# Kernel tuning notes

Measured on AMD Instinct MI355X. Metric: run time of the kernel, lower is better.

Reference implementation:

```python
import jax, jax.numpy as jnp
import numpy as np

DN = ('NCHW', 'OIHW', 'NCHW')

def conv3x3(x, w):
    # stride-1, SAME padding, no bias (matches build_conv_layer(..., 3, stride=1, padding='same', bias=False))
    return jax.lax.conv_general_dilated(x, w, window_strides=(1, 1), padding='SAME', dimension_numbers=DN)

def setup_inputs() -> dict:
    key = jax.random.key(0)
    k1, k2, k3, k4 = jax.random.split(key, 4)
    B, C, H, W = 4, 256, 64, 64
    inputs = jax.random.normal(k1, (B, C, H, W), dtype=jnp.float32)
    ref = jax.random.normal(k2, (B, C, H, W), dtype=jnp.float32)
    # xavier-uniform-ish conv weights, [O, I, kH, kW]
    fan = C * 9
    lim = np.sqrt(6.0 / (fan + fan)).astype(np.float32)
    w1 = jax.random.uniform(k3, (C, C, 3, 3), dtype=jnp.float32, minval=-lim, maxval=lim)
    w2 = jax.random.uniform(k4, (C, C, 3, 3), dtype=jnp.float32, minval=-lim, maxval=lim)
    gamma = jnp.float32(0.5)
    return {'inputs': inputs, 'ref': ref, 'w1': w1, 'w2': w2, 'gamma': gamma}

def reference(inputs, ref, w1, w2, gamma):
    # Faithful to source: x0 = relu(conv1(inputs)) is computed then immediately
    # overwritten by a view of x1 (a bug in the original), so inputs only
    # contributes its shape. We execute the dead conv for FLOP parity.
    _dead = jax.nn.relu(conv3x3(inputs, w1))
    x1 = jax.nn.relu(conv3x3(ref, w1))            # [B, C, H, W]
    B, C, H, W = x1.shape
    q = x1.transpose(0, 2, 3, 1).reshape(B, H * W, C)   # [B, HW, C]
    k = x1.reshape(B, C, H * W)                          # [B, C, HW]
    scores = jnp.einsum('bnc,bcm->bnm', q, k)            # [B, HW, HW]
    corr = jax.nn.softmax(scores, axis=1)                # softmax over dim=1 (atypical axis)
    v = jax.nn.relu(conv3x3(ref, w2)).reshape(B, C, H * W)  # [B, C, HW]
    A = jnp.einsum('bcn,bnm->bcm', v, corr).reshape(inputs.shape)
    return A * gamma + ref
```

## Files before the change

kernel.cpp:

```cpp
#include <hip/hip_runtime.h>
#include <math.h>

#define CDIM 256
#define NSEQ 4096
#define HWDIM 64
#define PPIX 4356

typedef unsigned short u16;
typedef __attribute__((ext_vector_type(8))) short bf16x8;
typedef __attribute__((ext_vector_type(4))) float f32x4;
typedef __attribute__((ext_vector_type(16))) float f32x16;

__device__ __forceinline__ u16 f2bf(float f) {
    unsigned u = __float_as_uint(f);
    unsigned r = (u + 0x7FFFu + ((u >> 16) & 1u)) >> 16;
    return (u16)r;
}

__device__ __forceinline__ void gload_lds16(const u16* g, u16* l) {
    __builtin_amdgcn_global_load_lds(
        (const __attribute__((address_space(1))) unsigned int*)g,
        (__attribute__((address_space(3))) unsigned int*)l, 16, 0, 0);
}

__global__ __launch_bounds__(256)
void pad_transpose_kernel(const float* __restrict__ x, u16* __restrict__ padded)
{
    __shared__ float lds[64 * 65];
    const int tid = threadIdx.x;
    const int y = blockIdx.x, c0 = blockIdx.y << 6, b = blockIdx.z;
    #pragma unroll
    for (int i = 0; i < 16; ++i) {
        int f = tid + (i << 8);
        int c = f >> 6, xx = f & 63;
        lds[c * 65 + xx] = x[(((size_t)(b * CDIM + c0 + c)) * HWDIM + y) * HWDIM + xx];
    }
    __syncthreads();
    #pragma unroll
    for (int i = 0; i < 2; ++i) {
        int f = tid + (i << 8);
        int xx = f >> 3, c8 = f & 7;
        union { u16 h[8]; float4 v; } pk;
        #pragma unroll
        for (int j = 0; j < 8; ++j) pk.h[j] = f2bf(lds[(c8 * 8 + j) * 65 + xx]);
        *(float4*)&padded[((size_t)b * PPIX + (y + 1) * 66 + (xx + 1)) * CDIM + c0 + (c8 << 3)] = pk.v;
    }
}

__global__ __launch_bounds__(256)
void w_prepack_kernel(const float* __restrict__ w, u16* __restrict__ wk)
{
    int t = (blockIdx.x << 8) + threadIdx.x;
    const float* wp = w + (size_t)t * 9;
    #pragma unroll
    for (int j = 0; j < 9; ++j) wk[j * 65536 + t] = f2bf(wp[j]);
}

template <bool OA>
__global__ __launch_bounds__(256)
void conv_mfma_kernel(const u16* __restrict__ padded, const u16* __restrict__ wk,
                      u16* __restrict__ out)
{
    __shared__ alignas(16) u16 Xs[64 * 64];
    __shared__ alignas(16) u16 Ws[128 * 64];

    const int tid = threadIdx.x;
    const int lane = tid & 63, wv = tid >> 6;
    const int lr = lane & 15, lg = lane >> 4;
    const int cb = blockIdx.x << 7;
    const int y0 = blockIdx.y;
    const int b = blockIdx.z;

    constexpr int MF = OA ? 4 : 2;
    constexpr int NF = OA ? 2 : 4;
    f32x4 acc[MF][NF] = {};

    for (int t = 0; t < 36; ++t) {
        const int kyx = t >> 2, cib = (t & 3) << 6;
        const int ky = kyx / 3, kx = kyx - ky * 3;
        __syncthreads();
        #pragma unroll
        for (int i = 0; i < 2; ++i) {
            int f = tid + (i << 8);
            int r = f >> 3, c8 = f & 7;
            int pp = (y0 + ky) * 66 + r + kx;
            float4 v = *(const float4*)&padded[((size_t)b * PPIX + pp) * CDIM + cib + (c8 << 3)];
            *(float4*)&Xs[(r << 6) + ((c8 << 3) ^ ((r & 7) << 3))] = v;
        }
        #pragma unroll
        for (int i = 0; i < 4; ++i) {
            int f = tid + (i << 8);
            int r = f >> 3, c8 = f & 7;
            float4 v = *(const float4*)&wk[((size_t)kyx << 16) + (size_t)(cb + r) * 256 + cib + (c8 << 3)];
            *(float4*)&Ws[(r << 6) + ((c8 << 3) ^ ((r & 7) << 3))] = v;
        }
        __syncthreads();
        #pragma unroll
        for (int kk = 0; kk < 2; ++kk) {
            const int ca = ((kk << 5) + (lg << 3)) ^ ((lr & 7) << 3);
            if constexpr (OA) {
                bf16x8 a[4], bb[2];
                #pragma unroll
                for (int mf = 0; mf < 4; ++mf)
                    a[mf] = *(const bf16x8*)&Xs[((mf * 16 + lr) << 6) + ca];
                #pragma unroll
                for (int nf = 0; nf < 2; ++nf)
                    bb[nf] = *(const bf16x8*)&Ws[((wv * 32 + nf * 16 + lr) << 6) + ca];
                #pragma unroll
                for (int mf = 0; mf < 4; ++mf)
                    #pragma unroll
                    for (int nf = 0; nf < 2; ++nf)
                        acc[mf][nf] = __builtin_amdgcn_mfma_f32_16x16x32_bf16(a[mf], bb[nf], acc[mf][nf], 0, 0, 0);
            } else {
                bf16x8 a[2], bb[4];
                #pragma unroll
                for (int mf = 0; mf < 2; ++mf)
                    a[mf] = *(const bf16x8*)&Ws[((wv * 32 + mf * 16 + lr) << 6) + ca];
                #pragma unroll
                for (int nf = 0; nf < 4; ++nf)
                    bb[nf] = *(const bf16x8*)&Xs[((nf * 16 + lr) << 6) + ca];
                #pragma unroll
                for (int mf = 0; mf < 2; ++mf)
                    #pragma unroll
                    for (int nf = 0; nf < 4; ++nf)
                        acc[mf][nf] = __builtin_amdgcn_mfma_f32_16x16x32_bf16(a[mf], bb[nf], acc[mf][nf], 0, 0, 0);
            }
        }
    }

    const int m0 = y0 << 6;
    if constexpr (OA) {
        #pragma unroll
        for (int mf = 0; mf < 4; ++mf)
            #pragma unroll
            for (int nf = 0; nf < 2; ++nf) {
                int nb = m0 + mf * 16 + lg * 4;
                int co = cb + wv * 32 + nf * 16 + lr;
                union { u16 h[4]; uint2 v; } pk;
                #pragma unroll
                for (int j = 0; j < 4; ++j) pk.h[j] = f2bf(fmaxf(acc[mf][nf][j], 0.f));
                *(uint2*)&out[((size_t)(b * CDIM + co)) * NSEQ + nb] = pk.v;
            }
    } else {
        #pragma unroll
        for (int mf = 0; mf < 2; ++mf)
            #pragma unroll
            for (int nf = 0; nf < 4; ++nf) {
                int cob = cb + wv * 32 + mf * 16 + lg * 4;
                int n = m0 + nf * 16 + lr;
                union { u16 h[4]; uint2 v; } pk;
                #pragma unroll
                for (int j = 0; j < 4; ++j) pk.h[j] = f2bf(fmaxf(acc[mf][nf][j], 0.f));
                *(uint2*)&out[((size_t)(b * NSEQ + n)) * CDIM + cob] = pk.v;
            }
    }
}

__global__ __launch_bounds__(256)
void rownorm_kernel(const u16* __restrict__ XT, float* __restrict__ rn2,
                    float* __restrict__ bmax)
{
    __shared__ float wmax[4];
    const int tid = threadIdx.x;
    const int lane = tid & 63, wv = tid >> 6;
    const int row = (blockIdx.x << 2) + wv;
    const u16* xp = &XT[(size_t)row * CDIM + (lane << 2)];
    uint2 v = *(const uint2*)xp;
    float s = 0.f;
    #pragma unroll
    for (int j = 0; j < 4; ++j) {
        unsigned hu = (j & 1) ? ((&v.x)[j >> 1] >> 16) : ((&v.x)[j >> 1] & 0xFFFFu);
        float x = __uint_as_float(hu << 16);
        s += x * x;
    }
    #pragma unroll
    for (int off = 1; off < 64; off <<= 1) s += __shfl_xor(s, off);
    if (lane == 0) {
        rn2[row] = s;
        wmax[wv] = s;
    }
    __syncthreads();
    if (tid == 0)
        bmax[blockIdx.x] = fmaxf(fmaxf(wmax[0], wmax[1]), fmaxf(wmax[2], wmax[3]));
}

__global__ __launch_bounds__(256)
void maxred_kernel(const float* __restrict__ bmax, float* __restrict__ maxrn2)
{
    __shared__ float wred[4];
    const int tid = threadIdx.x;
    const int lane = tid & 63, wv = tid >> 6;
    const int b = blockIdx.x;
    float m = 0.f;
    #pragma unroll
    for (int i = 0; i < 4; ++i)
        m = fmaxf(m, bmax[(b << 10) + (i << 8) + tid]);
    #pragma unroll
    for (int off = 1; off < 64; off <<= 1) m = fmaxf(m, __shfl_xor(m, off));
    if (lane == 0) wred[wv] = m;
    __syncthreads();
    if (tid == 0)
        maxrn2[b] = fmaxf(fmaxf(wred[0], wred[1]), fmaxf(wred[2], wred[3]));
}

#define M_TILE 128
#define NC 64
#define NCHUNKS 32

#define KS_OFF 0
#define VS_OFF 32768
#define P_OFF  65536

__device__ __forceinline__ void stage_chunk(const u16* __restrict__ XT, const u16* __restrict__ Vn,
                                            u16* Kb, u16* Vb, int b, int n0, int wv, int lane)
{
    #pragma unroll
    for (int i = 0; i < 4; ++i) {
        int f = ((i << 3) + wv) << 6;
        int fl = f + lane;
        int r = fl >> 5;
        int gsw = (fl & 31) ^ (r & 15);
        gload_lds16(&XT[(size_t)(b * NSEQ + n0 + r) * CDIM + (gsw << 3)], Kb + (f << 3));
    }
    #pragma unroll
    for (int i = 0; i < 4; ++i) {
        int f = ((i << 3) + wv) << 6;
        int fl = f + lane;
        int r = fl >> 3;
        int gsw = (fl & 7) ^ (r & 7);
        gload_lds16(&Vn[(size_t)(b * CDIM + r) * NSEQ + n0 + (gsw << 3)], Vb + (f << 3));
    }
}

__global__ __launch_bounds__(512, 2)
void attn_part_kernel(const u16* __restrict__ XT, const u16* __restrict__ Vn,
                      const float* __restrict__ rn2, const float* __restrict__ maxrn2,
                      float* __restrict__ o0, u16* __restrict__ o1,
                      float* __restrict__ lsum)
{
    __shared__ alignas(16) u16 smem[73728];
    u16* Ps = smem + P_OFF;

    const int tid = threadIdx.x;
    const int lane = tid & 63;
    const int wv = tid >> 6;
    const int l31 = lane & 31;
    const int hi = lane >> 5;
    const int bh = blockIdx.x;
    const int b = bh >> 1, h = bh & 1;
    const int m0 = blockIdx.y * M_TILE;
    const int nbase = h * (NSEQ / 2);

    const int qt = wv & 3;
    const int kh = wv >> 2;
    const int qa = qt * 32 + l31;
    const int qsel = wv & 1;
    const int csel = wv >> 1;

    const float mq = sqrtf(rn2[(size_t)b * NSEQ + m0 + qa]) * sqrtf(maxrn2[b]);

    bf16x8 qreg[16];
    {
        const u16* qrow = &XT[(size_t)(b * NSEQ + m0 + qa) * CDIM + (hi << 3)];
        #pragma unroll
        for (int ks = 0; ks < 16; ++ks)
            qreg[ks] = *(const bf16x8*)(qrow + (ks << 4));
    }

    f32x16 o[2][2] = {};
    float lrun = 0.f;

    stage_chunk(XT, Vn, smem + KS_OFF, smem + VS_OFF, b, nbase, wv, lane);
    __syncthreads();

    int cur = 0;
    for (int ci = 0; ci < NCHUNKS; ++ci) {
        if (ci + 1 < NCHUNKS)
            stage_chunk(XT, Vn, smem + KS_OFF + (cur ^ 1) * 16384,
                        smem + VS_OFF + (cur ^ 1) * 16384,
                        b, nbase + (ci + 1) * NC, wv, lane);

        const u16* Kc = smem + KS_OFF + cur * 16384;
        const u16* Vc = smem + VS_OFF + cur * 16384;

        f32x16 s = {};
        {
            const int krow = kh * 32 + l31;
            const u16* kbase = &Kc[krow << 8];
            const int ksw = krow & 15;
            #pragma unroll
            for (int ks = 0; ks < 16; ++ks) {
                bf16x8 ka = *(const bf16x8*)&kbase[(((ks << 1) + hi) ^ ksw) << 3];
                s = __builtin_amdgcn_mfma_f32_32x32x16_bf16(ka, qreg[ks], s, 0, 0, 0);
            }
        }

        float p[16];
        float ps = 0.f;
        #pragma unroll
        for (int r = 0; r < 16; ++r) { p[r] = __expf(s[r] - mq); ps += p[r]; }
        ps += __shfl_xor(ps, 32);
        lrun += ps;

        {
            const int swz = qa & 7;
            #pragma unroll
            for (int r4 = 0; r4 < 4; ++r4) {
                union { u16 h4[4]; uint2 v; } pk;
                pk.h4[0] = f2bf(p[r4 * 4 + 0]); pk.h4[1] = f2bf(p[r4 * 4 + 1]);
                pk.h4[2] = f2bf(p[r4 * 4 + 2]); pk.h4[3] = f2bf(p[r4 * 4 + 3]);
                int g = (kh << 2) + r4;
                *(uint2*)&Ps[(qa << 6) + (((g ^ swz) << 3) | (hi << 2))] = pk.v;
            }
        }
        __syncthreads();

        {
            const int q0 = ((qsel << 1) + 0) * 32 + l31;
            const int q1 = ((qsel << 1) + 1) * 32 + l31;
            const int c0 = ((csel << 1) + 0) * 32 + l31;
            const int c1 = ((csel << 1) + 1) * 32 + l31;
            #pragma unroll
            for (int ks = 0; ks < 4; ++ks) {
                const int gp = (ks << 1) + hi;
                bf16x8 pb0 = *(const bf16x8*)&Ps[(q0 << 6) + ((gp ^ (q0 & 7)) << 3)];
                bf16x8 pb1 = *(const bf16x8*)&Ps[(q1 << 6) + ((gp ^ (q1 & 7)) << 3)];
                bf16x8 va0 = *(const bf16x8*)&Vc[(c0 << 6) + ((gp ^ (c0 & 7)) << 3)];
                bf16x8 va1 = *(const bf16x8*)&Vc[(c1 << 6) + ((gp ^ (c1 & 7)) << 3)];
                o[0][0] = __builtin_amdgcn_mfma_f32_32x32x16_bf16(va0, pb0, o[0][0], 0, 0, 0);
                o[0][1] = __builtin_amdgcn_mfma_f32_32x32x16_bf16(va1, pb0, o[0][1], 0, 0, 0);
                o[1][0] = __builtin_amdgcn_mfma_f32_32x32x16_bf16(va0, pb1, o[1][0], 0, 0, 0);
                o[1][1] = __builtin_amdgcn_mfma_f32_32x32x16_bf16(va1, pb1, o[1][1], 0, 0, 0);
            }
        }

        __syncthreads();
        cur ^= 1;
    }

    if (lane < 32)
        lsum[(size_t)(((h * 2 + kh) * 4 + b)) * NSEQ + m0 + qa] = lrun;

    #pragma unroll
    for (int qi = 0; qi < 2; ++qi) {
        const int q = m0 + ((qsel << 1) + qi) * 32 + l31;
        #pragma unroll
        for (int cj = 0; cj < 2; ++cj) {
            #pragma unroll
            for (int reg = 0; reg < 16; ++reg) {
                int c = ((csel << 1) + cj) * 32 + (reg & 3) + ((reg >> 2) << 3) + (hi << 2);
                size_t oi = ((size_t)(b * CDIM + c)) * NSEQ + q;
                if (h == 0) o0[oi] = o[qi][cj][reg];
                else        o1[oi] = f2bf(o[qi][cj][reg]);
            }
        }
    }
}

__global__ __launch_bounds__(256)
void merge_kernel(float* __restrict__ out, const u16* __restrict__ o1,
                  const float* __restrict__ lsum, const float* __restrict__ ref,
                  const float* __restrict__ gptr)
{
    const int f = (blockIdx.x << 8) + threadIdx.x;
    const int n4 = f & 1023;
    const int c = (f >> 10) & 255;
    const int b = f >> 18;
    const float g = gptr[0];

    float4 p0 = ((const float4*)out)[f];
    uint2 q1 = *(const uint2*)&o1[((size_t)(b * CDIM + c)) * NSEQ + (n4 << 2)];
    float4 rf = ((const float4*)ref)[f];

    float res[4];
    #pragma unroll
    for (int j = 0; j < 4; ++j) {
        int row = (n4 << 2) + j;
        float l = lsum[(size_t)(0 * 4 + b) * NSEQ + row]
                + lsum[(size_t)(1 * 4 + b) * NSEQ + row]
                + lsum[(size_t)(2 * 4 + b) * NSEQ + row]
                + lsum[(size_t)(3 * 4 + b) * NSEQ + row];
        float rl = 1.0f / l;
        float v0 = ((const float*)&p0)[j];
        unsigned hu = ((j & 1) ? ((&q1.x)[j >> 1] >> 16) : ((&q1.x)[j >> 1] & 0xFFFFu));
        float v1 = __uint_as_float(hu << 16);
        float a = (v0 + v1) * rl;
        res[j] = g * a + ((const float*)&rf)[j];
    }
    ((float4*)out)[f] = *(float4*)res;
}

extern "C" void kernel_launch(void* const* d_in, const int* in_sizes, int n_in,
                              void* d_out, int out_size, void* d_ws, size_t ws_size,
                              hipStream_t stream)
{
    const float* ref = (const float*)d_in[1];
    const float* w1  = (const float*)d_in[2];
    const float* w2  = (const float*)d_in[3];
    const float* gma = (const float*)d_in[4];
    float* out = (float*)d_out;

    u16* XT     = (u16*)d_ws;
    u16* Vn     = XT + (size_t)4 * NSEQ * CDIM;
    u16* padded = Vn + (size_t)4 * NSEQ * CDIM;
    u16* wk1    = padded + (size_t)4 * PPIX * CDIM;
    u16* wk2    = wk1 + (size_t)9 * 65536;
    u16*   o1     = padded;
    float* lsum   = (float*)wk1;
    float* rn2    = (float*)wk2;
    float* bmax   = rn2 + 16384;
    float* maxrn2 = bmax + 4096;

    hipMemsetAsync(padded, 0, (size_t)4 * PPIX * CDIM * sizeof(u16), stream);
    pad_transpose_kernel<<<dim3(64, 4, 4), 256, 0, stream>>>(ref, padded);
    w_prepack_kernel<<<dim3(256), 256, 0, stream>>>(w1, wk1);
    w_prepack_kernel<<<dim3(256), 256, 0, stream>>>(w2, wk2);

    dim3 cgrid(2, 64, 4);
    conv_mfma_kernel<false><<<cgrid, 256, 0, stream>>>(padded, wk1, XT);
    conv_mfma_kernel<true ><<<cgrid, 256, 0, stream>>>(padded, wk2, Vn);

    rownorm_kernel<<<dim3(4096), 256, 0, stream>>>(XT, rn2, bmax);
    maxred_kernel<<<dim3(4), 256, 0, stream>>>(bmax, maxrn2);

    attn_part_kernel<<<dim3(8, NSEQ / M_TILE), 512, 0, stream>>>(XT, Vn, rn2, maxrn2, out, o1, lsum);
    merge_kernel<<<dim3((4 * CDIM * NSEQ / 4) / 256), 256, 0, stream>>>(out, o1, lsum, ref, gma);
}
```

Baseline: 181.8 us.

## Feed softmax probabilities to PV MFMA from registers via permlane swap

Score probabilities are packed to bf16 with v_cvt_pk_bf16_f32 and rearranged with v_permlane32_swap so they can serve directly as the B operand of the PV MFMA. This removes the LDS store/load of P and one barrier per chunk. Each wave now accumulates all 256 channels for its query/key slice, and the two key-half waves are summed through LDS once at the end. The cost is more accumulator registers (eight 32x32 tiles per wave) and more V reads from LDS per wave, which may pressure occupancy.

```diff
diff --git a/kernel.cpp b/kernel.cpp
--- a/kernel.cpp
+++ b/kernel.cpp
@@ -209,7 +209,6 @@
 
 #define KS_OFF 0
 #define VS_OFF 32768
-#define P_OFF  65536
 
 __device__ __forceinline__ void stage_chunk(const u16* __restrict__ XT, const u16* __restrict__ Vn,
                                             u16* Kb, u16* Vb, int b, int n0, int wv, int lane)
@@ -238,8 +237,7 @@
                       float* __restrict__ o0, u16* __restrict__ o1,
                       float* __restrict__ lsum)
 {
-    __shared__ alignas(16) u16 smem[73728];
-    u16* Ps = smem + P_OFF;
+    __shared__ alignas(16) u16 smem[65536];
 
     const int tid = threadIdx.x;
     const int lane = tid & 63;
@@ -254,8 +252,6 @@
     const int qt = wv & 3;
     const int kh = wv >> 2;
     const int qa = qt * 32 + l31;
-    const int qsel = wv & 1;
-    const int csel = wv >> 1;
 
     const float mq = sqrtf(rn2[(size_t)b * NSEQ + m0 + qa]) * sqrtf(maxrn2[b]);
 
@@ -267,7 +263,7 @@
             qreg[ks] = *(const bf16x8*)(qrow + (ks << 4));
     }
 
-    f32x16 o[2][2] = {};
+    f32x16 o[8] = {};
     float lrun = 0.f;
 
     stage_chunk(XT, Vn, smem + KS_OFF, smem + VS_OFF, b, nbase, wv, lane);
@@ -302,35 +298,28 @@
         ps += __shfl_xor(ps, 32);
         lrun += ps;
 
+        unsigned w[8];
+        #pragma unroll
+        for (int j = 0; j < 8; ++j)
+            asm("v_cvt_pk_bf16_f32 %0, %1, %2" : "=v"(w[j]) : "v"(p[2 * j]), "v"(p[2 * j + 1]));
+        asm volatile("v_permlane32_swap_b32 %0, %1" : "+v"(w[0]), "+v"(w[2]));
+        asm volatile("v_permlane32_swap_b32 %0, %1" : "+v"(w[1]), "+v"(w[3]));
+        asm volatile("v_permlane32_swap_b32 %0, %1" : "+v"(w[4]), "+v"(w[6]));
+        asm volatile("v_permlane32_swap_b32 %0, %1" : "+v"(w[5]), "+v"(w[7]));
+        union { unsigned u[4]; bf16x8 v; } pb0, pb1;
+        pb0.u[0] = w[0]; pb0.u[1] = w[1]; pb0.u[2] = w[2]; pb0.u[3] = w[3];
+        pb1.u[0] = w[4]; pb1.u[1] = w[5]; pb1.u[2] = w[6]; pb1.u[3] = w[7];
+
         {
-            const int swz = qa & 7;
-            #pragma unroll
-            for (int r4 = 0; r4 < 4; ++r4) {
-                union { u16 h4[4]; uint2 v; } pk;
-                pk.h4[0] = f2bf(p[r4 * 4 + 0]); pk.h4[1] = f2bf(p[r4 * 4 + 1]);
-                pk.h4[2] = f2bf(p[r4 * 4 + 2]); pk.h4[3] = f2bf(p[r4 * 4 + 3]);
-                int g = (kh << 2) + r4;
-                *(uint2*)&Ps[(qa << 6) + (((g ^ swz) << 3) | (hi << 2))] = pk.v;
-            }
-        }
-        __syncthreads();
-
-        {
-            const int q0 = ((qsel << 1) + 0) * 32 + l31;
-            const int q1 = ((qsel << 1) + 1) * 32 + l31;
-            const int c0 = ((csel << 1) + 0) * 32 + l31;
-            const int c1 = ((csel << 1) + 1) * 32 + l31;
-            #pragma unroll
-            for (int ks = 0; ks < 4; ++ks) {
-                const int gp = (ks << 1) + hi;
-                bf16x8 pb0 = *(const bf16x8*)&Ps[(q0 << 6) + ((gp ^ (q0 & 7)) << 3)];
-                bf16x8 pb1 = *(const bf16x8*)&Ps[(q1 << 6) + ((gp ^ (q1 & 7)) << 3)];
-                bf16x8 va0 = *(const bf16x8*)&Vc[(c0 << 6) + ((gp ^ (c0 & 7)) << 3)];
-                bf16x8 va1 = *(const bf16x8*)&Vc[(c1 << 6) + ((gp ^ (c1 & 7)) << 3)];
-                o[0][0] = __builtin_amdgcn_mfma_f32_32x32x16_bf16(va0, pb0, o[0][0], 0, 0, 0);
-                o[0][1] = __builtin_amdgcn_mfma_f32_32x32x16_bf16(va1, pb0, o[0][1], 0, 0, 0);
-                o[1][0] = __builtin_amdgcn_mfma_f32_32x32x16_bf16(va0, pb1, o[1][0], 0, 0, 0);
-                o[1][1] = __builtin_amdgcn_mfma_f32_32x32x16_bf16(va1, pb1, o[1][1], 0, 0, 0);
+            #pragma unroll
+            for (int cs = 0; cs < 8; ++cs) {
+                const int crow = cs * 32 + l31;
+                const int csw = (crow & 7);
+                const u16* vbase = &Vc[crow << 6];
+                bf16x8 va0 = *(const bf16x8*)&vbase[(((kh << 2) + 0 + hi) ^ csw) << 3];
+                bf16x8 va1 = *(const bf16x8*)&vbase[(((kh << 2) + 2 + hi) ^ csw) << 3];
+                o[cs] = __builtin_amdgcn_mfma_f32_32x32x16_bf16(va0, pb0.v, o[cs], 0, 0, 0);
+                o[cs] = __builtin_amdgcn_mfma_f32_32x32x16_bf16(va1, pb1.v, o[cs], 0, 0, 0);
             }
         }
 
@@ -341,19 +330,30 @@
     if (lane < 32)
         lsum[(size_t)(((h * 2 + kh) * 4 + b)) * NSEQ + m0 + qa] = lrun;
 
-    #pragma unroll
-    for (int qi = 0; qi < 2; ++qi) {
-        const int q = m0 + ((qsel << 1) + qi) * 32 + l31;
-        #pragma unroll
-        for (int cj = 0; cj < 2; ++cj) {
+    float* oq = (float*)smem + qt * 8192;
+    if (kh == 0) {
+        #pragma unroll
+        for (int cs = 0; cs < 8; ++cs)
             #pragma unroll
             for (int reg = 0; reg < 16; ++reg) {
-                int c = ((csel << 1) + cj) * 32 + (reg & 3) + ((reg >> 2) << 3) + (hi << 2);
+                int rloc = (reg & 3) + ((reg >> 2) << 3) + (hi << 2);
+                oq[((cs << 5) + rloc) * 32 + l31] = o[cs][reg];
+            }
+    }
+    __syncthreads();
+    if (kh == 1) {
+        #pragma unroll
+        for (int cs = 0; cs < 8; ++cs)
+            #pragma unroll
+            for (int reg = 0; reg < 16; ++reg) {
+                int rloc = (reg & 3) + ((reg >> 2) << 3) + (hi << 2);
+                float val = o[cs][reg] + oq[((cs << 5) + rloc) * 32 + l31];
+                int c = (cs << 5) + rloc;
+                int q = m0 + qt * 32 + l31;
                 size_t oi = ((size_t)(b * CDIM + c)) * NSEQ + q;
-                if (h == 0) o0[oi] = o[qi][cj][reg];
-                else        o1[oi] = f2bf(o[qi][cj][reg]);
-            }
-        }
+                if (h == 0) o0[oi] = val;
+                else        o1[oi] = f2bf(val);
+            }
     }
 }
 
```

Result: slower. 191.5 us (+5.3%).

## Double-buffer conv tiles via direct global-to-LDS loads; split attention MFMA chains

Applied to the files above, without the earlier changes.

The conv kernel now stages its input and weight tiles with global_load_lds into double-buffered shared memory. The next tile is prefetched while MFMAs run on the current one, and the swizzle moves to the global address side. In the attention kernel, the QK^T MFMA chain is split into two independent accumulators to shorten the dependency chain, and s_setprio raises wave priority around the MFMA loops. The costs are more LDS per block (48KB for conv) and an extra vector add per chunk.

```diff
diff --git a/kernel.cpp b/kernel.cpp
--- a/kernel.cpp
+++ b/kernel.cpp
@@ -56,13 +56,40 @@
     for (int j = 0; j < 9; ++j) wk[j * 65536 + t] = f2bf(wp[j]);
 }
 
+__device__ __forceinline__ void conv_stage(const u16* __restrict__ padded,
+                                           const u16* __restrict__ wk,
+                                           u16* Xb, u16* Wb,
+                                           int b, int y0, int cb, int t,
+                                           int wv, int lane)
+{
+    const int kyx = t >> 2, cib = (t & 3) << 6;
+    const int ky = kyx / 3, kx = kyx - ky * 3;
+    #pragma unroll
+    for (int i = 0; i < 2; ++i) {
+        int f = ((i << 2) + wv) << 6;
+        int fl = f + lane;
+        int r = fl >> 3;
+        int gsw = (fl & 7) ^ (r & 7);
+        gload_lds16(&padded[((size_t)b * PPIX + (y0 + ky) * 66 + r + kx) * CDIM + cib + (gsw << 3)],
+                    Xb + (f << 3));
+    }
+    #pragma unroll
+    for (int i = 0; i < 4; ++i) {
+        int f = ((i << 2) + wv) << 6;
+        int fl = f + lane;
+        int r = fl >> 3;
+        int gsw = (fl & 7) ^ (r & 7);
+        gload_lds16(&wk[((size_t)kyx << 16) + (size_t)(cb + r) * 256 + cib + (gsw << 3)],
+                    Wb + (f << 3));
+    }
+}
+
 template <bool OA>
 __global__ __launch_bounds__(256)
 void conv_mfma_kernel(const u16* __restrict__ padded, const u16* __restrict__ wk,
                       u16* __restrict__ out)
 {
-    __shared__ alignas(16) u16 Xs[64 * 64];
-    __shared__ alignas(16) u16 Ws[128 * 64];
+    __shared__ alignas(16) u16 smem[24576];
 
     const int tid = threadIdx.x;
     const int lane = tid & 63, wv = tid >> 6;
@@ -75,26 +102,18 @@
     constexpr int NF = OA ? 2 : 4;
     f32x4 acc[MF][NF] = {};
 
+    conv_stage(padded, wk, smem, smem + 8192, b, y0, cb, 0, wv, lane);
+    __syncthreads();
+
+    int cur = 0;
     for (int t = 0; t < 36; ++t) {
-        const int kyx = t >> 2, cib = (t & 3) << 6;
-        const int ky = kyx / 3, kx = kyx - ky * 3;
-        __syncthreads();
-        #pragma unroll
-        for (int i = 0; i < 2; ++i) {
-            int f = tid + (i << 8);
-            int r = f >> 3, c8 = f & 7;
-            int pp = (y0 + ky) * 66 + r + kx;
-            float4 v = *(const float4*)&padded[((size_t)b * PPIX + pp) * CDIM + cib + (c8 << 3)];
-            *(float4*)&Xs[(r << 6) + ((c8 << 3) ^ ((r & 7) << 3))] = v;
-        }
-        #pragma unroll
-        for (int i = 0; i < 4; ++i) {
-            int f = tid + (i << 8);
-            int r = f >> 3, c8 = f & 7;
-            float4 v = *(const float4*)&wk[((size_t)kyx << 16) + (size_t)(cb + r) * 256 + cib + (c8 << 3)];
-            *(float4*)&Ws[(r << 6) + ((c8 << 3) ^ ((r & 7) << 3))] = v;
-        }
-        __syncthreads();
+        if (t + 1 < 36)
+            conv_stage(padded, wk, smem + (cur ^ 1) * 4096,
+                       smem + 8192 + (cur ^ 1) * 8192, b, y0, cb, t + 1, wv, lane);
+
+        const u16* Xs = smem + cur * 4096;
+        const u16* Ws = smem + 8192 + cur * 8192;
+
         #pragma unroll
         for (int kk = 0; kk < 2; ++kk) {
             const int ca = ((kk << 5) + (lg << 3)) ^ ((lr & 7) << 3);
@@ -126,6 +145,8 @@
                         acc[mf][nf] = __builtin_amdgcn_mfma_f32_16x16x32_bf16(a[mf], bb[nf], acc[mf][nf], 0, 0, 0);
             }
         }
+        __syncthreads();
+        cur ^= 1;
     }
 
     const int m0 = y0 << 6;
@@ -283,17 +304,22 @@
         const u16* Kc = smem + KS_OFF + cur * 16384;
         const u16* Vc = smem + VS_OFF + cur * 16384;
 
-        f32x16 s = {};
+        f32x16 s0 = {}, s1 = {};
         {
             const int krow = kh * 32 + l31;
             const u16* kbase = &Kc[krow << 8];
             const int ksw = krow & 15;
-            #pragma unroll
-            for (int ks = 0; ks < 16; ++ks) {
-                bf16x8 ka = *(const bf16x8*)&kbase[(((ks << 1) + hi) ^ ksw) << 3];
-                s = __builtin_amdgcn_mfma_f32_32x32x16_bf16(ka, qreg[ks], s, 0, 0, 0);
-            }
+            __builtin_amdgcn_s_setprio(1);
+            #pragma unroll
+            for (int ks = 0; ks < 16; ks += 2) {
+                bf16x8 ka0 = *(const bf16x8*)&kbase[((((ks + 0) << 1) + hi) ^ ksw) << 3];
+                bf16x8 ka1 = *(const bf16x8*)&kbase[((((ks + 1) << 1) + hi) ^ ksw) << 3];
+                s0 = __builtin_amdgcn_mfma_f32_32x32x16_bf16(ka0, qreg[ks], s0, 0, 0, 0);
+                s1 = __builtin_amdgcn_mfma_f32_32x32x16_bf16(ka1, qreg[ks + 1], s1, 0, 0, 0);
+            }
+            __builtin_amdgcn_s_setprio(0);
         }
+        f32x16 s = s0 + s1;
 
         float p[16];
         float ps = 0.f;
@@ -320,6 +346,7 @@
             const int q1 = ((qsel << 1) + 1) * 32 + l31;
             const int c0 = ((csel << 1) + 0) * 32 + l31;
             const int c1 = ((csel << 1) + 1) * 32 + l31;
+            __builtin_amdgcn_s_setprio(1);
             #pragma unroll
             for (int ks = 0; ks < 4; ++ks) {
                 const int gp = (ks << 1) + hi;
@@ -332,6 +359,7 @@
                 o[1][0] = __builtin_amdgcn_mfma_f32_32x32x16_bf16(va0, pb1, o[1][0], 0, 0, 0);
                 o[1][1] = __builtin_amdgcn_mfma_f32_32x32x16_bf16(va1, pb1, o[1][1], 0, 0, 0);
             }
+            __builtin_amdgcn_s_setprio(0);
         }
 
         __syncthreads();
```

New measurement: 168.8 us. 1.08x faster.
